# Kernel tuning notes

Hardware: AMD Instinct MI355X
Metric: run time of the kernel (lower is better)

The kernel has to match this reference:

```python
import jax, jax.numpy as jnp
import numpy as np

VOL = 128
FACTOR = 0.5 * VOL
N = 262144
LAT = 16
B = 8


def setup_inputs() -> dict:
    key = jax.random.key(0)
    ks = jax.random.split(key, 10)
    x = jax.random.normal(ks[0], (B, LAT), jnp.float32)
    inds = jax.random.randint(ks[1], (N, 3), 1, 126, dtype=jnp.int32)
    reference_values = jax.random.normal(ks[2], (N,), jnp.float32)
    # SIREN first layer: U(-1/in, 1/in)
    W0 = jax.random.uniform(ks[3], (LAT, 8), jnp.float32, -1.0 / LAT, 1.0 / LAT)
    b0 = jnp.zeros((8,), jnp.float32)
    # SIREN hidden layers (4 residual layers): U(-sqrt(6/in), sqrt(6/in))
    lim_h = float(np.sqrt(6.0 / 8.0))
    Wh = jax.random.uniform(ks[4], (4, 8, 8), jnp.float32, -lim_h, lim_h)
    bh = jnp.zeros((4, 8), jnp.float32)
    # final glorot-uniform layer: 8 -> 4N
    lim_f = float(np.sqrt(6.0 / (8.0 + 4.0 * N)))
    Wf = jax.random.uniform(ks[5], (8, 4 * N), jnp.float32, -lim_f, lim_f)
    bf = jnp.zeros((4 * N,), jnp.float32)
    return {"x": x, "W0": W0, "b0": b0, "Wh": Wh, "bh": bh, "Wf": Wf,
            "bf": bf, "reference_values": reference_values, "inds": inds}


def _siren_mlp(x, W0, b0, Wh, bh, Wf, bf):
    bf16 = jnp.bfloat16
    h = jnp.sin(30.0 * (x.astype(bf16) @ W0.astype(bf16) + b0.astype(bf16)))
    for i in range(Wh.shape[0]):  # 4 residual sine layers, 8-wide
        h = h + jnp.sin(h @ Wh[i].astype(bf16) + bh[i].astype(bf16))
    return h.astype(jnp.float32) @ Wf + bf  # [B, 4N], final layer in fp32


def reference(x, W0, b0, Wh, bh, Wf, bf, reference_values, inds):
    Bn = x.shape[0]
    out = _siren_mlp(x, W0, b0, Wh, bh, Wf, bf).reshape(Bn, N, 4)
    delta_coords, delta_values = out[..., :3], out[..., 3]
    # coords = stack(z,y,x reversed) normalized to [-1,1)
    coords_norm = (jnp.stack([inds[:, 2], inds[:, 1], inds[:, 0]], axis=1)
                   .astype(jnp.float32) - FACTOR) / FACTOR  # [N,3]
    values = reference_values + delta_values                 # [B,N]
    coords = FACTOR * (coords_norm[None] + delta_coords) + FACTOR  # [B,N,3]
    bposf = jnp.floor(coords)
    bposi = bposf.astype(jnp.int32)
    f = coords - bposf
    fx, fy, fz = f[..., 0], f[..., 1], f[..., 2]
    gx, gy, gz = 1.0 - fx, 1.0 - fy, 1.0 - fz
    # 8 trilinear weights, in the original concat order
    w = jnp.stack([gx * gy * gz, fx * gy * gz, gx * fy * gz, gx * gy * fz,
                   gx * fy * fz, fx * gy * fz, fx * fy * gz, fx * fy * fz],
                  axis=1)                                    # [B,8,N]
    bamp = (values[:, None, :] * w).reshape(Bn, 8 * N)
    offs = jnp.array([[0, 0, 0], [1, 0, 0], [0, 1, 0], [0, 0, 1],
                      [0, 1, 1], [1, 0, 1], [1, 1, 0], [1, 1, 1]], jnp.int32)
    bpos = (bposi[:, None, :, :] + offs[None, :, None, :]).reshape(Bn, 8 * N, 3)

    def scatter(pos, amp):
        return jnp.zeros((VOL, VOL, VOL), jnp.float32).at[
            pos[:, 2], pos[:, 1], pos[:, 0]].add(amp)

    grids = jax.vmap(scatter)(bpos, bamp)  # [B,128,128,128]
    return grids
```

## Files before the change

kernel.cpp:

```cpp
#include <hip/hip_runtime.h>
#include <hip/hip_fp16.h>
#include <math.h>
#include <string.h>

#define VOL   128
#define V2    (VOL*VOL)
#define V3    (VOL*VOL*VOL)
#define NPTS  262144
#define LATD  16
#define BATCH 8
#define FACTORF 64.0f
#define NBINS (VOL*VOL)
#define RZ 8
#define RY 8
#define HALO 13
#define NRANGE (HALO*HALO)
#define TBL_CAP 4096
#define FAR_CAP 8192

#define WS_HBUF   0u
#define WS_HIST   256u
#define WS_START  65792u
#define WS_RANK   131344u
#define WS_CTRL   1179920u
#define WS_FARBUF 1179952u
#define WS_COORDC 1311024u
#define WS_FULL   18088240u

__device__ __forceinline__ float bf16r(float x) {
    unsigned u = __float_as_uint(x);
    u = (u + 0x7fffu + ((u >> 16) & 1u)) & 0xffff0000u;
    return __uint_as_float(u);
}
__device__ __forceinline__ unsigned short f16bits(float v) {
    __half h = __float2half_rn(v);
    unsigned short us; memcpy(&us, &h, 2);
    return us;
}
__device__ __forceinline__ float f16val(unsigned short us) {
    __half h; memcpy(&h, &us, 2);
    return __half2float(h);
}

__global__ void mlp_kernel(const float* __restrict__ x,
                           const float* __restrict__ W0,
                           const float* __restrict__ b0,
                           const float* __restrict__ Wh,
                           const float* __restrict__ bh,
                           float* __restrict__ hout) {
    int b = threadIdx.x;
    if (b >= BATCH) return;
    float xb[LATD];
    #pragma unroll
    for (int i = 0; i < LATD; ++i) xb[i] = bf16r(x[b*LATD + i]);
    float h[8];
    #pragma unroll
    for (int j = 0; j < 8; ++j) {
        float acc = 0.f;
        #pragma unroll
        for (int i = 0; i < LATD; ++i) acc += xb[i] * bf16r(W0[i*8 + j]);
        float t = bf16r(acc);
        t = bf16r(t + bf16r(b0[j]));
        t = bf16r(30.0f * t);
        h[j] = bf16r(sinf(t));
    }
    for (int l = 0; l < 4; ++l) {
        float nh[8];
        #pragma unroll
        for (int j = 0; j < 8; ++j) {
            float acc = 0.f;
            #pragma unroll
            for (int r = 0; r < 8; ++r) acc += h[r] * bf16r(Wh[(l*8 + r)*8 + j]);
            float t = bf16r(acc);
            t = bf16r(t + bf16r(bh[l*8 + j]));
            float s = bf16r(sinf(t));
            nh[j] = bf16r(h[j] + s);
        }
        #pragma unroll
        for (int j = 0; j < 8; ++j) h[j] = nh[j];
    }
    #pragma unroll
    for (int j = 0; j < 8; ++j) hout[b*8 + j] = h[j];
}

__global__ __launch_bounds__(256) void hist_rank_kernel(const int* __restrict__ inds,
                                                        unsigned* __restrict__ hist,
                                                        unsigned* __restrict__ rank) {
    int n = blockIdx.x * 256 + threadIdx.x;
    if (n >= NPTS) return;
    rank[n] = atomicAdd(&hist[inds[n*3]*VOL + inds[n*3+1]], 1u);
}

__global__ __launch_bounds__(256) void scan_kernel(const unsigned* __restrict__ hist,
                                                   unsigned* __restrict__ binstart,
                                                   unsigned* __restrict__ ctrl) {
    __shared__ unsigned part[256];
    int t = threadIdx.x;
    const int CH = NBINS / 256;
    unsigned s = 0;
    for (int k = 0; k < CH; ++k) s += hist[t*CH + k];
    part[t] = s; __syncthreads();
    for (int off = 1; off < 256; off <<= 1) {
        unsigned v = (t >= off) ? part[t - off] : 0u;
        __syncthreads();
        part[t] += v;
        __syncthreads();
    }
    unsigned run = (t == 0) ? 0u : part[t - 1];
    for (int k = 0; k < CH; ++k) {
        int idx = t*CH + k;
        binstart[idx] = run;
        run += hist[idx];
    }
    if (t == 0) { binstart[NBINS] = NPTS; ctrl[0] = 0u; ctrl[1] = 0u; }
}

__global__ __launch_bounds__(256) void coords_kernel(
    const float* __restrict__ Wf, const float* __restrict__ bfv_g,
    const float* __restrict__ rv, const int* __restrict__ inds,
    const float* __restrict__ hbuf, const unsigned* __restrict__ binstart,
    const unsigned* __restrict__ rank,
    unsigned* __restrict__ ctrl, float4* __restrict__ farbuf,
    ushort4* __restrict__ coords_c)
{
    __shared__ float hs[64];
    if (threadIdx.x < 64) hs[threadIdx.x] = hbuf[threadIdx.x];
    __syncthreads();
    int n = blockIdx.x * 256 + threadIdx.x;
    if (n >= NPTS) return;
    int iz = inds[n*3], iy = inds[n*3+1], ix = inds[n*3+2];
    float cnx = ((float)ix - FACTORF) / FACTORF;
    float cny = ((float)iy - FACTORF) / FACTORF;
    float cnz = ((float)iz - FACTORF) / FACTORF;
    float val0 = rv[n];
    float4 bfv = ((const float4*)bfv_g)[n];
    float4 wf[8];
    #pragma unroll
    for (int r = 0; r < 8; ++r)
        wf[r] = ((const float4*)(Wf + (size_t)r * 4 * NPTS))[n];
    unsigned pos = binstart[iz*VOL + iy] + rank[n];
    #pragma unroll
    for (int b = 0; b < BATCH; ++b) {
        float o0 = bfv.x, o1 = bfv.y, o2 = bfv.z, o3 = bfv.w;
        #pragma unroll
        for (int r = 0; r < 8; ++r) {
            float hv = hs[b*8 + r];
            o0 = fmaf(hv, wf[r].x, o0);
            o1 = fmaf(hv, wf[r].y, o1);
            o2 = fmaf(hv, wf[r].z, o2);
            o3 = fmaf(hv, wf[r].w, o3);
        }
        float cx = FACTORF * (cnx + o0) + FACTORF;
        float cy = FACTORF * (cny + o1) + FACTORF;
        float cz = FACTORF * (cnz + o2) + FACTORF;
        float val = val0 + o3;
        int bz = (int)floorf(cz), by = (int)floorf(cy);
        bool nearzy = ((unsigned)(bz - iz + 2) <= 4u) &&
                      ((unsigned)(by - iy + 2) <= 4u);
        ushort4 e;
        if (nearzy) {
            e.x = (unsigned short)fminf(fmaxf(fmaf(cx + 8.f, 256.f, 0.5f), 0.f), 65535.f);
            e.y = (unsigned short)fminf(fmaf(cy - (float)iy + 2.f, 8192.f, 0.5f), 40959.f);
            e.z = (unsigned short)fminf(fmaf(cz - (float)iz + 2.f, 8192.f, 0.5f), 40959.f);
            e.w = f16bits(val);
        } else {
            e.x = 0; e.y = 0xFFFFu; e.z = 0; e.w = 0;
            unsigned fp = atomicAdd(&ctrl[0], 1u);
            if (fp < FAR_CAP)
                farbuf[fp] = make_float4(cx, cy, cz + 256.0f * (float)b, val);
        }
        coords_c[(size_t)b * NPTS + pos] = e;
    }
}

__global__ __launch_bounds__(256) void region_kernel(
    const ushort4* __restrict__ coords_c,
    const unsigned* __restrict__ binstart, float* __restrict__ out)
{
    __shared__ float tile[RZ*RY*VOL];
    __shared__ unsigned tbl[TBL_CAP];
    __shared__ unsigned rcum[NRANGE+1];
    __shared__ int rbase[NRANGE];
    int tid = threadIdx.x;
    int b   = blockIdx.x >> 8;
    int rid = blockIdx.x & 255;
    int z0 = (rid >> 4) * RZ, y0 = (rid & 15) * RY;

    for (int i = tid; i < RZ*RY*VOL; i += 256) tile[i] = 0.f;

    unsigned rs = 0;
    if (tid < NRANGE) {
        int zi = tid / HALO, yi = tid - zi * HALO;
        int zz = (z0 - 3 + zi) & (VOL-1);
        int yy = (y0 - 3 + yi) & (VOL-1);
        int base = zz * VOL + yy;
        rs = binstart[base];
        rcum[tid+1] = binstart[base+1] - rs;
    }
    if (tid == 0) rcum[0] = 0u;
    __syncthreads();
    for (int off = 1; off < NRANGE; off <<= 1) {
        unsigned v = 0u;
        if (tid < NRANGE && tid >= off) v = rcum[tid+1-off];
        __syncthreads();
        if (tid < NRANGE && tid >= off) rcum[tid+1] += v;
        __syncthreads();
    }
    if (tid < NRANGE) rbase[tid] = (int)rs - (int)rcum[tid];
    __syncthreads();

    unsigned total = rcum[NRANGE];
    const ushort4* cb = coords_c + (size_t)b * NPTS;
    const int ox[8] = {0,1,0,0,0,1,1,1};
    const int oy[8] = {0,0,1,0,1,0,1,1};
    const int oz[8] = {0,0,0,1,1,1,0,1};

    for (unsigned c0 = 0; c0 < total; c0 += TBL_CAP) {
        unsigned c1 = (total - c0 < TBL_CAP) ? total : c0 + TBL_CAP;
        __syncthreads();
        if (tid < NRANGE) {
            unsigned lo = rcum[tid] > c0 ? rcum[tid] : c0;
            unsigned hi = rcum[tid+1] < c1 ? rcum[tid+1] : c1;
            int zi = tid / HALO, yi = tid - zi * HALO;
            unsigned meta = ((unsigned)zi << 22) | ((unsigned)yi << 26);
            int rb = rbase[tid];
            for (unsigned i = lo; i < hi; ++i)
                tbl[i - c0] = (unsigned)(rb + (int)i) | meta;
        }
        __syncthreads();
        unsigned nn = c1 - c0;
        for (unsigned f = tid; f < nn; f += 2048u) {
            ushort4 e[8]; unsigned t[8]; bool v[8];
            #pragma unroll
            for (int u = 0; u < 8; ++u) {
                unsigned fu = f + (unsigned)u * 256u;
                v[u] = fu < nn;
                if (v[u]) {
                    t[u] = tbl[fu];
                    e[u] = cb[t[u] & 0x3FFFFFu];
                }
            }
            #pragma unroll
            for (int u = 0; u < 8; ++u) {
                if (!v[u] || e[u].y == 0xFFFFu) continue;
                int zi = (int)((t[u] >> 22) & 15u), yi = (int)((t[u] >> 26) & 15u);
                int piz = (z0 - 3 + zi) & (VOL-1);
                int piy = (y0 - 3 + yi) & (VOL-1);
                float cx = (float)e[u].x * (1.f/256.f) - 8.f;
                float cy = (float)piy + (float)e[u].y * (1.f/8192.f) - 2.f;
                float cz = (float)piz + (float)e[u].z * (1.f/8192.f) - 2.f;
                float val = f16val(e[u].w);
                float fxf = floorf(cx), fyf = floorf(cy), fzf = floorf(cz);
                int bx = (int)fxf, by = (int)fyf, bz = (int)fzf;
                float fx = cx - fxf, fy = cy - fyf, fz = cz - fzf;
                float gx = 1.f - fx, gy = 1.f - fy, gz = 1.f - fz;
                float w[8] = {gx*gy*gz, fx*gy*gz, gx*fy*gz, gx*gy*fz,
                              gx*fy*fz, fx*gy*fz, fx*fy*gz, fx*fy*fz};
                #pragma unroll
                for (int o = 0; o < 8; ++o) {
                    int Z = (bz + oz[o]) & (VOL-1), dz = Z - z0;
                    if ((unsigned)dz >= RZ) continue;
                    int Y = (by + oy[o]) & (VOL-1), dy = Y - y0;
                    if ((unsigned)dy >= RY) continue;
                    int X = (bx + ox[o]) & (VOL-1);
                    atomicAdd(&tile[(dz << 10) + (dy << 7) + X], val * w[o]);
                }
            }
        }
    }
    __syncthreads();
    size_t ob = (size_t)b * V3;
    for (int i = tid; i < RZ*RY*VOL; i += 256) {
        int lz = i >> 10, ly = (i >> 7) & (RY-1), lx = i & 127;
        out[ob + (size_t)(z0+lz)*V2 + (y0+ly)*VOL + lx] = tile[i];
    }
}

__global__ __launch_bounds__(256) void far_kernel(
    const unsigned* __restrict__ ctrl, const float4* __restrict__ farbuf,
    float* __restrict__ out)
{
    unsigned cnt = ctrl[0];
    if (cnt > FAR_CAP) cnt = FAR_CAP;
    const int ox[8] = {0,1,0,0,0,1,1,1};
    const int oy[8] = {0,0,1,0,1,0,1,1};
    const int oz[8] = {0,0,0,1,1,1,0,1};
    for (unsigned idx = blockIdx.x * 256 + threadIdx.x; idx < cnt;
         idx += gridDim.x * 256) {
        float4 c = farbuf[idx];
        int b = (int)floorf((c.z + 8.0f) * (1.0f/256.0f));
        float cz = c.z - 256.0f * (float)b;
        float fxf = floorf(c.x), fyf = floorf(c.y), fzf = floorf(cz);
        int bx = (int)fxf, by = (int)fyf, bz = (int)fzf;
        float fx = c.x - fxf, fy = c.y - fyf, fz = cz - fzf;
        float gx = 1.f - fx, gy = 1.f - fy, gz = 1.f - fz;
        float val = c.w;
        float w[8] = {gx*gy*gz, fx*gy*gz, gx*fy*gz, gx*gy*fz,
                      gx*fy*fz, fx*gy*fz, fx*fy*gz, fx*fy*fz};
        float* ob = out + (size_t)b * V3;
        #pragma unroll
        for (int o = 0; o < 8; ++o) {
            int Z = (bz + oz[o]) & (VOL-1);
            int Y = (by + oy[o]) & (VOL-1);
            int X = (bx + ox[o]) & (VOL-1);
            atomicAdd(ob + (size_t)Z*V2 + Y*VOL + X, val * w[o]);
        }
    }
}

__global__ __launch_bounds__(256) void scatter_fallback(
    const float* __restrict__ Wf, const float* __restrict__ bfv_g,
    const float* __restrict__ rv, const int* __restrict__ inds,
    const float* __restrict__ hbuf, float* __restrict__ out)
{
    __shared__ float hs[BATCH*8];
    if (threadIdx.x < BATCH*8) hs[threadIdx.x] = hbuf[threadIdx.x];
    __syncthreads();
    int n = blockIdx.x * blockDim.x + threadIdx.x;
    if (n >= NPTS) return;
    int iz = inds[n*3 + 0], iy = inds[n*3 + 1], ix = inds[n*3 + 2];
    float cnx = ((float)ix - FACTORF) / FACTORF;
    float cny = ((float)iy - FACTORF) / FACTORF;
    float cnz = ((float)iz - FACTORF) / FACTORF;
    float val0 = rv[n];
    float4 bfv = ((const float4*)bfv_g)[n];
    float4 wf[8];
    #pragma unroll
    for (int r = 0; r < 8; ++r)
        wf[r] = ((const float4*)(Wf + (size_t)r * 4 * NPTS))[n];
    static const int offs[8][3] = {{0,0,0},{1,0,0},{0,1,0},{0,0,1},
                                   {0,1,1},{1,0,1},{1,1,0},{1,1,1}};
    #pragma unroll
    for (int b = 0; b < BATCH; ++b) {
        float o0 = bfv.x, o1 = bfv.y, o2 = bfv.z, o3 = bfv.w;
        #pragma unroll
        for (int r = 0; r < 8; ++r) {
            float hv = hs[b*8 + r];
            o0 = fmaf(hv, wf[r].x, o0);
            o1 = fmaf(hv, wf[r].y, o1);
            o2 = fmaf(hv, wf[r].z, o2);
            o3 = fmaf(hv, wf[r].w, o3);
        }
        float cx = FACTORF * (cnx + o0) + FACTORF;
        float cy = FACTORF * (cny + o1) + FACTORF;
        float cz = FACTORF * (cnz + o2) + FACTORF;
        float val = val0 + o3;
        float fxf = floorf(cx), fyf = floorf(cy), fzf = floorf(cz);
        int bx = (int)fxf, by = (int)fyf, bz = (int)fzf;
        float fx = cx - fxf, fy = cy - fyf, fz = cz - fzf;
        float gx = 1.f - fx, gy = 1.f - fy, gz = 1.f - fz;
        float w[8] = {gx*gy*gz, fx*gy*gz, gx*fy*gz, gx*gy*fz,
                      gx*fy*fz, fx*gy*fz, fx*fy*gz, fx*fy*fz};
        float* ob = out + (size_t)b * V3;
        #pragma unroll
        for (int o = 0; o < 8; ++o) {
            int X = (bx + offs[o][0]) & (VOL-1);
            int Y = (by + offs[o][1]) & (VOL-1);
            int Z = (bz + offs[o][2]) & (VOL-1);
            atomicAdd(ob + (size_t)Z*V2 + Y*VOL + X, val * w[o]);
        }
    }
}

extern "C" void kernel_launch(void* const* d_in, const int* in_sizes, int n_in,
                              void* d_out, int out_size, void* d_ws, size_t ws_size,
                              hipStream_t stream) {
    const float* x    = (const float*)d_in[0];
    const float* W0   = (const float*)d_in[1];
    const float* b0   = (const float*)d_in[2];
    const float* Wh   = (const float*)d_in[3];
    const float* bh   = (const float*)d_in[4];
    const float* Wf   = (const float*)d_in[5];
    const float* bf   = (const float*)d_in[6];
    const float* rv   = (const float*)d_in[7];
    const int*   inds = (const int*)d_in[8];
    float* out = (float*)d_out;
    char*  ws  = (char*)d_ws;

    float*    hbuf     = (float*)(ws + WS_HBUF);
    unsigned* hist     = (unsigned*)(ws + WS_HIST);
    unsigned* binstart = (unsigned*)(ws + WS_START);
    unsigned* rank     = (unsigned*)(ws + WS_RANK);
    unsigned* ctrl     = (unsigned*)(ws + WS_CTRL);
    float4*   farbuf   = (float4*)(ws + WS_FARBUF);
    ushort4*  coords_c = (ushort4*)(ws + WS_COORDC);

    mlp_kernel<<<1, 64, 0, stream>>>(x, W0, b0, Wh, bh, hbuf);

    if (ws_size >= (size_t)WS_FULL) {
        hipMemsetAsync(hist, 0, NBINS*4, stream);
        hist_rank_kernel<<<NPTS/256, 256, 0, stream>>>(inds, hist, rank);
        scan_kernel<<<1, 256, 0, stream>>>(hist, binstart, ctrl);
        coords_kernel<<<NPTS/256, 256, 0, stream>>>(Wf, bf, rv, inds, hbuf,
                                                    binstart, rank,
                                                    ctrl, farbuf, coords_c);
        region_kernel<<<256*BATCH, 256, 0, stream>>>(coords_c, binstart, out);
        far_kernel<<<8, 256, 0, stream>>>(ctrl, farbuf, out);
    } else {
        hipMemsetAsync(d_out, 0, (size_t)out_size * sizeof(float), stream);
        scatter_fallback<<<NPTS/256, 256, 0, stream>>>(Wf, bf, rv, inds, hbuf, out);
    }
}
```

Baseline: 188.1 us.

## Interleave batches in sorted coords buffer and process 4 batches per region block

The compressed coordinate buffer changes from batch-major to point-major, so each sorted point's 8 batch entries sit contiguously. Each region block now handles 4 batches over a smaller 8x4 tile, reading 32 bytes per point and dropping the shared index table in favour of a per-thread range walk. An early reject skips points whose 2x2 footprint misses the tile. The single-block scan is also split into a three-kernel parallel scan. The aim is fewer redundant halo gathers and better coalescing, at the cost of more kernel launches and a larger halo ratio with RY=4.

```diff
diff --git a/kernel.cpp b/kernel.cpp
--- a/kernel.cpp
+++ b/kernel.cpp
@@ -12,10 +12,11 @@
 #define FACTORF 64.0f
 #define NBINS (VOL*VOL)
 #define RZ 8
-#define RY 8
-#define HALO 13
-#define NRANGE (HALO*HALO)
-#define TBL_CAP 4096
+#define RY 4
+#define BG 4
+#define HALO_Z (RZ+5)
+#define HALO_Y (RY+5)
+#define NRANGE (HALO_Z*HALO_Y)
 #define FAR_CAP 8192
 
 #define WS_HBUF   0u
@@ -23,22 +24,24 @@
 #define WS_START  65792u
 #define WS_RANK   131344u
 #define WS_CTRL   1179920u
-#define WS_FARBUF 1179952u
-#define WS_COORDC 1311024u
-#define WS_FULL   18088240u
+#define WS_WGSUM  1179952u
+#define WS_FARBUF 1180208u
+#define WS_COORDC 1311280u
+#define WS_FULL   18088496u
 
 __device__ __forceinline__ float bf16r(float x) {
     unsigned u = __float_as_uint(x);
     u = (u + 0x7fffu + ((u >> 16) & 1u)) & 0xffff0000u;
     return __uint_as_float(u);
 }
-__device__ __forceinline__ unsigned short f16bits(float v) {
+__device__ __forceinline__ unsigned f16bits(float v) {
     __half h = __float2half_rn(v);
     unsigned short us; memcpy(&us, &h, 2);
-    return us;
-}
-__device__ __forceinline__ float f16val(unsigned short us) {
-    __half h; memcpy(&h, &us, 2);
+    return (unsigned)us;
+}
+__device__ __forceinline__ float f16val(unsigned us) {
+    unsigned short u16 = (unsigned short)us;
+    __half h; memcpy(&h, &u16, 2);
     return __half2float(h);
 }
 
@@ -91,28 +94,43 @@
     rank[n] = atomicAdd(&hist[inds[n*3]*VOL + inds[n*3+1]], 1u);
 }
 
-__global__ __launch_bounds__(256) void scan_kernel(const unsigned* __restrict__ hist,
+__global__ __launch_bounds__(256) void scanA_kernel(const unsigned* __restrict__ hist,
+                                                    unsigned* __restrict__ wgsum) {
+    __shared__ unsigned s[256];
+    int t = threadIdx.x;
+    s[t] = hist[blockIdx.x * 256 + t];
+    __syncthreads();
+    for (int off = 128; off > 0; off >>= 1) {
+        if (t < off) s[t] += s[t + off];
+        __syncthreads();
+    }
+    if (t == 0) wgsum[blockIdx.x] = s[0];
+}
+__global__ __launch_bounds__(64) void scanB_kernel(unsigned* __restrict__ wgsum,
                                                    unsigned* __restrict__ binstart,
                                                    unsigned* __restrict__ ctrl) {
-    __shared__ unsigned part[256];
+    if (threadIdx.x == 0) {
+        unsigned run = 0;
+        for (int i = 0; i < 64; ++i) { unsigned v = wgsum[i]; wgsum[i] = run; run += v; }
+        binstart[NBINS] = run;
+        ctrl[0] = 0u; ctrl[1] = 0u;
+    }
+}
+__global__ __launch_bounds__(256) void scanC_kernel(const unsigned* __restrict__ hist,
+                                                    const unsigned* __restrict__ wgsum,
+                                                    unsigned* __restrict__ binstart) {
+    __shared__ unsigned s[256];
     int t = threadIdx.x;
-    const int CH = NBINS / 256;
-    unsigned s = 0;
-    for (int k = 0; k < CH; ++k) s += hist[t*CH + k];
-    part[t] = s; __syncthreads();
+    int idx = blockIdx.x * 256 + t;
+    unsigned h = hist[idx];
+    s[t] = h; __syncthreads();
     for (int off = 1; off < 256; off <<= 1) {
-        unsigned v = (t >= off) ? part[t - off] : 0u;
+        unsigned v = (t >= off) ? s[t - off] : 0u;
         __syncthreads();
-        part[t] += v;
+        s[t] += v;
         __syncthreads();
     }
-    unsigned run = (t == 0) ? 0u : part[t - 1];
-    for (int k = 0; k < CH; ++k) {
-        int idx = t*CH + k;
-        binstart[idx] = run;
-        run += hist[idx];
-    }
-    if (t == 0) { binstart[NBINS] = NPTS; ctrl[0] = 0u; ctrl[1] = 0u; }
+    binstart[idx] = s[t] - h + wgsum[blockIdx.x];
 }
 
 __global__ __launch_bounds__(256) void coords_kernel(
@@ -121,7 +139,7 @@
     const float* __restrict__ hbuf, const unsigned* __restrict__ binstart,
     const unsigned* __restrict__ rank,
     unsigned* __restrict__ ctrl, float4* __restrict__ farbuf,
-    ushort4* __restrict__ coords_c)
+    uint4* __restrict__ coords_c)
 {
     __shared__ float hs[64];
     if (threadIdx.x < 64) hs[threadIdx.x] = hbuf[threadIdx.x];
@@ -139,6 +157,7 @@
     for (int r = 0; r < 8; ++r)
         wf[r] = ((const float4*)(Wf + (size_t)r * 4 * NPTS))[n];
     unsigned pos = binstart[iz*VOL + iy] + rank[n];
+    unsigned ew[16];
     #pragma unroll
     for (int b = 0; b < BATCH; ++b) {
         float o0 = bfv.x, o1 = bfv.y, o2 = bfv.z, o3 = bfv.w;
@@ -157,45 +176,50 @@
         int bz = (int)floorf(cz), by = (int)floorf(cy);
         bool nearzy = ((unsigned)(bz - iz + 2) <= 4u) &&
                       ((unsigned)(by - iy + 2) <= 4u);
-        ushort4 e;
         if (nearzy) {
-            e.x = (unsigned short)fminf(fmaxf(fmaf(cx + 8.f, 256.f, 0.5f), 0.f), 65535.f);
-            e.y = (unsigned short)fminf(fmaf(cy - (float)iy + 2.f, 8192.f, 0.5f), 40959.f);
-            e.z = (unsigned short)fminf(fmaf(cz - (float)iz + 2.f, 8192.f, 0.5f), 40959.f);
-            e.w = f16bits(val);
+            unsigned ex = (unsigned)fminf(fmaxf(fmaf(cx + 8.f, 256.f, 0.5f), 0.f), 65535.f);
+            unsigned ey = (unsigned)fminf(fmaf(cy - (float)iy + 2.f, 8192.f, 0.5f), 40959.f);
+            unsigned ez = (unsigned)fminf(fmaf(cz - (float)iz + 2.f, 8192.f, 0.5f), 40959.f);
+            ew[b*2]   = ex | (ey << 16);
+            ew[b*2+1] = ez | (f16bits(val) << 16);
         } else {
-            e.x = 0; e.y = 0xFFFFu; e.z = 0; e.w = 0;
+            ew[b*2]   = 0xFFFF0000u;
+            ew[b*2+1] = 0u;
             unsigned fp = atomicAdd(&ctrl[0], 1u);
             if (fp < FAR_CAP)
                 farbuf[fp] = make_float4(cx, cy, cz + 256.0f * (float)b, val);
         }
-        coords_c[(size_t)b * NPTS + pos] = e;
-    }
+    }
+    uint4* dst = coords_c + (size_t)pos * 4;
+    #pragma unroll
+    for (int k = 0; k < 4; ++k)
+        dst[k] = make_uint4(ew[k*4], ew[k*4+1], ew[k*4+2], ew[k*4+3]);
 }
 
 __global__ __launch_bounds__(256) void region_kernel(
-    const ushort4* __restrict__ coords_c,
+    const uint4* __restrict__ coords_c,
     const unsigned* __restrict__ binstart, float* __restrict__ out)
 {
-    __shared__ float tile[RZ*RY*VOL];
-    __shared__ unsigned tbl[TBL_CAP];
+    __shared__ float tile[BG*RZ*RY*VOL];
+    __shared__ unsigned rstart[NRANGE];
     __shared__ unsigned rcum[NRANGE+1];
-    __shared__ int rbase[NRANGE];
+    __shared__ short rpz[NRANGE], rpy[NRANGE];
     int tid = threadIdx.x;
-    int b   = blockIdx.x >> 8;
-    int rid = blockIdx.x & 255;
-    int z0 = (rid >> 4) * RZ, y0 = (rid & 15) * RY;
-
-    for (int i = tid; i < RZ*RY*VOL; i += 256) tile[i] = 0.f;
-
-    unsigned rs = 0;
+    int bg  = blockIdx.x >> 9;
+    int rid = blockIdx.x & 511;
+    int z0 = (rid >> 5) * RZ, y0 = (rid & 31) * RY;
+
+    for (int i = tid; i < BG*RZ*RY*VOL; i += 256) tile[i] = 0.f;
+
     if (tid < NRANGE) {
-        int zi = tid / HALO, yi = tid - zi * HALO;
+        int zi = tid / HALO_Y, yi = tid - zi * HALO_Y;
         int zz = (z0 - 3 + zi) & (VOL-1);
         int yy = (y0 - 3 + yi) & (VOL-1);
         int base = zz * VOL + yy;
-        rs = binstart[base];
-        rcum[tid+1] = binstart[base+1] - rs;
+        unsigned s = binstart[base];
+        rstart[tid] = s;
+        rpz[tid] = (short)zz; rpy[tid] = (short)yy;
+        rcum[tid+1] = binstart[base+1] - s;
     }
     if (tid == 0) rcum[0] = 0u;
     __syncthreads();
@@ -206,73 +230,76 @@
         if (tid < NRANGE && tid >= off) rcum[tid+1] += v;
         __syncthreads();
     }
-    if (tid < NRANGE) rbase[tid] = (int)rs - (int)rcum[tid];
-    __syncthreads();
-
     unsigned total = rcum[NRANGE];
-    const ushort4* cb = coords_c + (size_t)b * NPTS;
+
     const int ox[8] = {0,1,0,0,0,1,1,1};
     const int oy[8] = {0,0,1,0,1,0,1,1};
     const int oz[8] = {0,0,0,1,1,1,0,1};
 
-    for (unsigned c0 = 0; c0 < total; c0 += TBL_CAP) {
-        unsigned c1 = (total - c0 < TBL_CAP) ? total : c0 + TBL_CAP;
-        __syncthreads();
-        if (tid < NRANGE) {
-            unsigned lo = rcum[tid] > c0 ? rcum[tid] : c0;
-            unsigned hi = rcum[tid+1] < c1 ? rcum[tid+1] : c1;
-            int zi = tid / HALO, yi = tid - zi * HALO;
-            unsigned meta = ((unsigned)zi << 22) | ((unsigned)yi << 26);
-            int rb = rbase[tid];
-            for (unsigned i = lo; i < hi; ++i)
-                tbl[i - c0] = (unsigned)(rb + (int)i) | meta;
-        }
-        __syncthreads();
-        unsigned nn = c1 - c0;
-        for (unsigned f = tid; f < nn; f += 2048u) {
-            ushort4 e[8]; unsigned t[8]; bool v[8];
+    int r = 0;
+    for (unsigned f = tid; f < total; f += 512u) {
+        uint4 qa[2], qb[2]; int pz[2], py[2]; bool v[2];
+        #pragma unroll
+        for (int u = 0; u < 2; ++u) {
+            unsigned fu = f + (unsigned)u * 256u;
+            v[u] = fu < total;
+            if (v[u]) {
+                while (fu >= rcum[r+1]) ++r;
+                unsigned j = rstart[r] + (fu - rcum[r]);
+                const uint4* src = coords_c + (size_t)j * 4 + (size_t)bg * 2;
+                qa[u] = src[0];
+                qb[u] = src[1];
+                pz[u] = rpz[r]; py[u] = rpy[r];
+            }
+        }
+        #pragma unroll
+        for (int u = 0; u < 2; ++u) {
+            if (!v[u]) continue;
+            int piz = pz[u], piy = py[u];
+            unsigned w0[4] = {qa[u].x, qa[u].z, qb[u].x, qb[u].z};
+            unsigned w1[4] = {qa[u].y, qa[u].w, qb[u].y, qb[u].w};
             #pragma unroll
-            for (int u = 0; u < 8; ++u) {
-                unsigned fu = f + (unsigned)u * 256u;
-                v[u] = fu < nn;
-                if (v[u]) {
-                    t[u] = tbl[fu];
-                    e[u] = cb[t[u] & 0x3FFFFFu];
-                }
-            }
-            #pragma unroll
-            for (int u = 0; u < 8; ++u) {
-                if (!v[u] || e[u].y == 0xFFFFu) continue;
-                int zi = (int)((t[u] >> 22) & 15u), yi = (int)((t[u] >> 26) & 15u);
-                int piz = (z0 - 3 + zi) & (VOL-1);
-                int piy = (y0 - 3 + yi) & (VOL-1);
-                float cx = (float)e[u].x * (1.f/256.f) - 8.f;
-                float cy = (float)piy + (float)e[u].y * (1.f/8192.f) - 2.f;
-                float cz = (float)piz + (float)e[u].z * (1.f/8192.f) - 2.f;
-                float val = f16val(e[u].w);
+            for (int e = 0; e < 4; ++e) {
+                unsigned lo = w0[e], hi = w1[e];
+                unsigned ey = lo >> 16;
+                if (ey == 0xFFFFu) continue;
+                unsigned ez = hi & 0xFFFFu;
+                int bz = piz + (int)(ez >> 13) - 2;
+                int by = piy + (int)(ey >> 13) - 2;
+                int dz0 = (bz - z0) & 127, dz1 = (bz + 1 - z0) & 127;
+                if (dz0 >= RZ && dz1 >= RZ) continue;
+                int dy0 = (by - y0) & 127, dy1 = (by + 1 - y0) & 127;
+                if (dy0 >= RY && dy1 >= RY) continue;
+                float cx = (float)(lo & 0xFFFFu) * (1.f/256.f) - 8.f;
+                float cy = (float)piy + (float)ey * (1.f/8192.f) - 2.f;
+                float cz = (float)piz + (float)ez * (1.f/8192.f) - 2.f;
+                float val = f16val(hi >> 16);
                 float fxf = floorf(cx), fyf = floorf(cy), fzf = floorf(cz);
-                int bx = (int)fxf, by = (int)fyf, bz = (int)fzf;
+                int bx = (int)fxf;
                 float fx = cx - fxf, fy = cy - fyf, fz = cz - fzf;
                 float gx = 1.f - fx, gy = 1.f - fy, gz = 1.f - fz;
                 float w[8] = {gx*gy*gz, fx*gy*gz, gx*fy*gz, gx*gy*fz,
                               gx*fy*fz, fx*gy*fz, fx*fy*gz, fx*fy*fz};
+                float* tb = tile + (e << 12);
                 #pragma unroll
                 for (int o = 0; o < 8; ++o) {
-                    int Z = (bz + oz[o]) & (VOL-1), dz = Z - z0;
-                    if ((unsigned)dz >= RZ) continue;
-                    int Y = (by + oy[o]) & (VOL-1), dy = Y - y0;
-                    if ((unsigned)dy >= RY) continue;
-                    int X = (bx + ox[o]) & (VOL-1);
-                    atomicAdd(&tile[(dz << 10) + (dy << 7) + X], val * w[o]);
+                    int dz = (bz + oz[o] - z0) & 127;
+                    if (dz >= RZ) continue;
+                    int dy = (by + oy[o] - y0) & 127;
+                    if (dy >= RY) continue;
+                    int X = (bx + ox[o]) & 127;
+                    atomicAdd(&tb[(dz << 9) + (dy << 7) + X], val * w[o]);
                 }
             }
         }
     }
     __syncthreads();
-    size_t ob = (size_t)b * V3;
-    for (int i = tid; i < RZ*RY*VOL; i += 256) {
-        int lz = i >> 10, ly = (i >> 7) & (RY-1), lx = i & 127;
-        out[ob + (size_t)(z0+lz)*V2 + (y0+ly)*VOL + lx] = tile[i];
+    for (int i = tid; i < BG*RZ*RY*VOL; i += 256) {
+        int bgl = i >> 12;
+        int rem = i & 4095;
+        int lz = rem >> 9, ly = (rem >> 7) & (RY-1), lx = rem & 127;
+        out[(size_t)(bg*BG + bgl) * V3 + (size_t)(z0+lz)*V2 + (y0+ly)*VOL + lx]
+            = tile[i];
     }
 }
 
@@ -382,19 +409,22 @@
     unsigned* binstart = (unsigned*)(ws + WS_START);
     unsigned* rank     = (unsigned*)(ws + WS_RANK);
     unsigned* ctrl     = (unsigned*)(ws + WS_CTRL);
+    unsigned* wgsum    = (unsigned*)(ws + WS_WGSUM);
     float4*   farbuf   = (float4*)(ws + WS_FARBUF);
-    ushort4*  coords_c = (ushort4*)(ws + WS_COORDC);
+    uint4*    coords_c = (uint4*)(ws + WS_COORDC);
 
     mlp_kernel<<<1, 64, 0, stream>>>(x, W0, b0, Wh, bh, hbuf);
 
     if (ws_size >= (size_t)WS_FULL) {
         hipMemsetAsync(hist, 0, NBINS*4, stream);
         hist_rank_kernel<<<NPTS/256, 256, 0, stream>>>(inds, hist, rank);
-        scan_kernel<<<1, 256, 0, stream>>>(hist, binstart, ctrl);
+        scanA_kernel<<<64, 256, 0, stream>>>(hist, wgsum);
+        scanB_kernel<<<1, 64, 0, stream>>>(wgsum, binstart, ctrl);
+        scanC_kernel<<<64, 256, 0, stream>>>(hist, wgsum, binstart);
         coords_kernel<<<NPTS/256, 256, 0, stream>>>(Wf, bf, rv, inds, hbuf,
                                                     binstart, rank,
                                                     ctrl, farbuf, coords_c);
-        region_kernel<<<256*BATCH, 256, 0, stream>>>(coords_c, binstart, out);
+        region_kernel<<<512*(BATCH/BG), 256, 0, stream>>>(coords_c, binstart, out);
         far_kernel<<<8, 256, 0, stream>>>(ctrl, farbuf, out);
     } else {
         hipMemsetAsync(d_out, 0, (size_t)out_size * sizeof(float), stream);
```

After: 176.2 us. 1.07x faster.
